# Kernel optimization log

Measured on AMD Instinct MI355X. Metric: run time of the kernel, lower is better.

Reference implementation:

```python
import jax, jax.numpy as jnp
import numpy as np
from jax import lax

EPS = 1e-5
W_BITS = 8
A_BITS = 8


def _ste_round(x):
    # straight-through round (brevitas-style)
    return x + lax.stop_gradient(jnp.round(x) - x)


def weight_fake_quant(w, bits=W_BITS):
    # symmetric per-output-channel int quant: scale = max|w| / (2^(b-1)-1)
    qmax = float(2 ** (bits - 1) - 1)
    s = jnp.max(jnp.abs(w), axis=(1, 2, 3), keepdims=True) / qmax
    s = jnp.maximum(s, 1e-8)
    return jnp.clip(_ste_round(w / s), -qmax, qmax) * s


def quant_relu(x, scale, bits=A_BITS):
    # QuantReLU: relu then unsigned fake-quant with learned per-tensor scale
    qmax = float(2 ** bits - 1)
    s = jnp.maximum(scale, 1e-6)
    return jnp.clip(_ste_round(jax.nn.relu(x) / s), 0.0, qmax) * s


def conv2d(x, w, stride=1, padding=0):
    return lax.conv_general_dilated(
        x, w, window_strides=(stride, stride),
        padding=[(padding, padding), (padding, padding)],
        dimension_numbers=('NCHW', 'OIHW', 'NCHW'))


def batchnorm(x, gamma, beta, mean, var):
    # eval-mode BN with running stats
    inv = gamma / jnp.sqrt(var + EPS)
    return x * inv[None, :, None, None] + (beta - mean * inv)[None, :, None, None]


def setup_inputs() -> dict:
    key = jax.random.key(0)
    ks = jax.random.split(key, 20)
    B, Cin, P, H, W = 64, 1024, 256, 14, 14
    inp = {
        'x': jax.random.normal(ks[0], (B, Cin, H, W), jnp.float32),
        'w1': jax.random.normal(ks[1], (P, Cin, 1, 1), jnp.float32) * 0.05,
        'w2': jax.random.normal(ks[2], (P, P, 3, 3), jnp.float32) * 0.05,
        'w3': jax.random.normal(ks[3], (Cin, P, 1, 1), jnp.float32) * 0.05,
        'bn1_gamma': jax.random.uniform(ks[4], (P,), jnp.float32, 0.5, 1.5),
        'bn1_beta': jax.random.normal(ks[5], (P,), jnp.float32) * 0.1,
        'bn1_mean': jax.random.normal(ks[6], (P,), jnp.float32) * 0.1,
        'bn1_var': jax.random.uniform(ks[7], (P,), jnp.float32, 0.5, 1.5),
        'bn2_gamma': jax.random.uniform(ks[8], (P,), jnp.float32, 0.5, 1.5),
        'bn2_beta': jax.random.normal(ks[9], (P,), jnp.float32) * 0.1,
        'bn2_mean': jax.random.normal(ks[10], (P,), jnp.float32) * 0.1,
        'bn2_var': jax.random.uniform(ks[11], (P,), jnp.float32, 0.5, 1.5),
        'bn3_gamma': jax.random.uniform(ks[12], (Cin,), jnp.float32, 0.5, 1.5),
        'bn3_beta': jax.random.normal(ks[13], (Cin,), jnp.float32) * 0.1,
        'bn3_mean': jax.random.normal(ks[14], (Cin,), jnp.float32) * 0.1,
        'bn3_var': jax.random.uniform(ks[15], (Cin,), jnp.float32, 0.5, 1.5),
        's1': jax.random.uniform(ks[16], (1,), jnp.float32, 0.02, 0.1),
        's2': jax.random.uniform(ks[17], (1,), jnp.float32, 0.02, 0.1),
        's3': jax.random.uniform(ks[18], (1,), jnp.float32, 0.02, 0.1),
    }
    return inp


def reference(x, w1, w2, w3,
              bn1_gamma, bn1_beta, bn1_mean, bn1_var,
              bn2_gamma, bn2_beta, bn2_mean, bn2_var,
              bn3_gamma, bn3_beta, bn3_mean, bn3_var,
              s1, s2, s3):
    identity = x
    out = conv2d(x, weight_fake_quant(w1))
    out = batchnorm(out, bn1_gamma, bn1_beta, bn1_mean, bn1_var)
    out = quant_relu(out, s1)
    out = conv2d(out, weight_fake_quant(w2), stride=1, padding=1)
    out = batchnorm(out, bn2_gamma, bn2_beta, bn2_mean, bn2_var)
    out = quant_relu(out, s2)
    out = conv2d(out, weight_fake_quant(w3))
    out = batchnorm(out, bn3_gamma, bn3_beta, bn3_mean, bn3_var)
    out = out + identity  # downsample=None -> identity skip
    out = quant_relu(out, s3)
    return out
```

## Files before the change

kernel.cpp:

```cpp
#include <hip/hip_runtime.h>
#include <stdint.h>
#include <stddef.h>

typedef unsigned short u16;
typedef unsigned int   u32;
typedef signed char    s8;
typedef int   i32x4 __attribute__((ext_vector_type(4)));
typedef float f32x4 __attribute__((ext_vector_type(4)));
typedef s8    s8x4  __attribute__((ext_vector_type(4)));
typedef u32   u32x4 __attribute__((ext_vector_type(4)));

#define DEVFN static __device__ __forceinline__

#define GLL(g, l) __builtin_amdgcn_global_load_lds( \
    (__attribute__((address_space(1))) void*)(g),   \
    (__attribute__((address_space(3))) void*)(l), 16, 0, 0)

#define NREAL 12544
#define NPAD  16384
#define GUARD_ROWS 32
#define SXI 4096.0f

DEVFN float blockReduceMax(float m) {
    for (int off = 32; off; off >>= 1) m = fmaxf(m, __shfl_xor(m, off));
    __shared__ float s[4];
    int lane = threadIdx.x & 63, w = threadIdx.x >> 6;
    if (lane == 0) s[w] = m;
    __syncthreads();
    return fmaxf(fmaxf(s[0], s[1]), fmaxf(s[2], s[3]));
}
DEVFN float blockReduceSum(float v) {
    for (int off = 32; off; off >>= 1) v += __shfl_xor(v, off);
    __shared__ float s[4];
    int lane = threadIdx.x & 63, w = threadIdx.x >> 6;
    __syncthreads();
    if (lane == 0) s[w] = v;
    __syncthreads();
    return s[0] + s[1] + s[2] + s[3];
}

__global__ __launch_bounds__(256) void k_prep(
    const float* __restrict__ w1, const float* __restrict__ w2, const float* __restrict__ w3,
    const float* __restrict__ x,
    const float* __restrict__ g1, const float* __restrict__ b1, const float* __restrict__ m1, const float* __restrict__ v1,
    const float* __restrict__ g2, const float* __restrict__ b2, const float* __restrict__ m2, const float* __restrict__ v2,
    const float* __restrict__ g3, const float* __restrict__ b3, const float* __restrict__ m3, const float* __restrict__ v3,
    const float* __restrict__ s1p, const float* __restrict__ s2p,
    s8* __restrict__ w1q8, s8* __restrict__ w2t8, s8* __restrict__ w3q8,
    float* __restrict__ a1, float* __restrict__ c1,
    float* __restrict__ a2, float* __restrict__ c2,
    float* __restrict__ a3, float* __restrict__ c3,
    s8* __restrict__ xq, s8* __restrict__ act1g)
{
    __shared__ float tile[64*197];
    const int bid = blockIdx.x, t = threadIdx.x;

    if (bid < 256) {
        int p = bid;
        const float* wr = w1 + (size_t)p * 1024;
        float v[4], mx = 0.f;
        for (int i = 0; i < 4; ++i) { v[i] = wr[t + i*256]; mx = fmaxf(mx, fabsf(v[i])); }
        mx = blockReduceMax(mx);
        float s = fmaxf(mx / 127.0f, 1e-8f);
        float qs = 0.f;
        for (int i = 0; i < 4; ++i) {
            float q = fminf(fmaxf(rintf(v[i] / s), -127.f), 127.f);
            s8 qb = (s8)(int)q;
            w1q8[(size_t)p*2048 + t + i*256]        = qb;
            w1q8[(size_t)p*2048 + 1024 + t + i*256] = qb;
            qs += q;
        }
        qs = blockReduceSum(qs);
        if (t == 0) {
            float s1 = fmaxf(s1p[0], 1e-6f);
            float inv = g1[p] / sqrtf(v1[p] + 1e-5f);
            float a = s * (1.0f / SXI) * inv / s1;
            a1[p] = a;
            c1[p] = (b1[p] - m1[p] * inv) / s1 + 128.0f * qs * a;
        }
    } else if (bid < 512) {
        int p = bid - 256;
        const float* wr = w2 + (size_t)p * 2304;
        float v[9], mx = 0.f;
        for (int i = 0; i < 9; ++i) { v[i] = wr[t + i*256]; mx = fmaxf(mx, fabsf(v[i])); }
        mx = blockReduceMax(mx);
        float s = fmaxf(mx / 127.0f, 1e-8f);
        float qs = 0.f;
        for (int i = 0; i < 9; ++i) {
            int f = t + i*256;
            int ci = f / 9, r = f - ci*9;
            float q = fminf(fmaxf(rintf(v[i] / s), -127.f), 127.f);
            w2t8[(size_t)p*2304 + r*256 + ci] = (s8)(int)q;
            qs += q;
        }
        qs = blockReduceSum(qs);
        if (t == 0) {
            float s1 = fmaxf(s1p[0], 1e-6f), s2 = fmaxf(s2p[0], 1e-6f);
            float inv = g2[p] / sqrtf(v2[p] + 1e-5f);
            float a = s * s1 * inv / s2;
            a2[p] = a;
            c2[p] = (b2[p] - m2[p] * inv) / s2 + 128.0f * qs * a;
        }
    } else if (bid < 1536) {
        int co = bid - 512;
        float v = w3[(size_t)co*256 + t];
        float mx = blockReduceMax(fabsf(v));
        float s = fmaxf(mx / 127.0f, 1e-8f);
        float q = fminf(fmaxf(rintf(v / s), -127.f), 127.f);
        w3q8[(size_t)co*256 + t] = (s8)(int)q;
        float qs = blockReduceSum(q);
        if (t == 0) {
            float s2 = fmaxf(s2p[0], 1e-6f);
            float inv = g3[co] / sqrtf(v3[co] + 1e-5f);
            float a = s * s2 * inv;
            a3[co] = a;
            c3[co] = (b3[co] - m3[co] * inv) + 128.0f * qs * a;
        }
    } else if (bid < 2560) {
        int sb = bid - 1536;
        int b = sb >> 4, cg = sb & 15;
        const float* xb = x + ((size_t)b*1024 + cg*64) * 196;
        for (int i = t; i < 3136; i += 256) {
            f32x4 v = *(const f32x4*)&xb[i*4];
            int g = i*4;
#pragma unroll
            for (int j = 0; j < 4; ++j) {
                int gg = g + j;
                tile[gg + gg/196] = v[j];
            }
        }
        __syncthreads();
        for (int i = t; i < 3136; i += 256) {
            int pos = i >> 4, c4 = (i & 15) << 2;
            s8x4 hi, lo;
#pragma unroll
            for (int j = 0; j < 4; ++j) {
                float v = tile[(c4 + j)*197 + pos];
                int xf = (int)rintf(v * SXI);
                xf = xf > 32767 ? 32767 : (xf < -32767 ? -32767 : xf);
                int h = xf >> 8;
                int l = xf - (h << 8) - 128;
                hi[j] = (s8)h;
                lo[j] = (s8)l;
            }
            size_t n = (size_t)(b*196 + pos);
            *(s8x4*)&xq[n*2048 + cg*64 + c4]        = hi;
            *(s8x4*)&xq[n*2048 + 1024 + cg*64 + c4] = lo;
        }
    } else {
        const int total16 = (NPAD + 2*GUARD_ROWS) * 256 / 16;
        u32x4 val; val[0] = val[1] = val[2] = val[3] = 0x80808080u;
        u32x4* dst = (u32x4*)act1g;
        for (int i = (bid - 2560)*256 + t; i < total16; i += 260*256) dst[i] = val;
    }
}

template<int CONV>
__global__ __launch_bounds__(256) void k_gemm(
    const s8* __restrict__ A, const s8* __restrict__ Bact,
    s8* __restrict__ actout,
    const float* __restrict__ ca, const float* __restrict__ cc,
    const float* __restrict__ xin, const float* __restrict__ s3p,
    float* __restrict__ outp)
{
    constexpr int KSA = CONV==1 ? 2048 : (CONV==2 ? 2304 : 256);
    constexpr int KSB = CONV==1 ? 2048 : 256;
    constexpr int NKT = CONV==1 ? 16 : (CONV==2 ? 18 : 2);

    __shared__ s8 lA[3][128*128];
    __shared__ s8 lB[3][64*128];

    const int t = threadIdx.x;
    const int lane = t & 63, wv = t >> 6;
    const int n0 = blockIdx.x * 64, m0 = blockIdx.y * 128;

    i32x4 acc[4][2], accB[4][2];
#pragma unroll
    for (int i = 0; i < 4; ++i)
#pragma unroll
        for (int j = 0; j < 2; ++j) { acc[i][j] = i32x4{0,0,0,0}; accB[i][j] = i32x4{0,0,0,0}; }

    const int srA = wv*32 + (lane >> 3);
    const int srB = wv*16 + (lane >> 3);
    const int ssel = (((lane & 7) ^ ((lane >> 3) & 7))) * 16;
    const int wr = wv >> 1, wc = wv & 1;
    const int fr = lane & 15, fg = lane >> 4;
    const int fsw = (fr & 7) << 4;

    auto stageK = [&](int kt, int buf) {
        int bcol, bshift;
        if constexpr (CONV == 2) {
            bcol = (kt & 1) * 128;
            int kpos = kt >> 1;
            int ky = kpos / 3, kx = kpos - ky*3;
            bshift = (ky - 1)*16 + (kx - 1);
        } else { bcol = kt * 128; bshift = 0; }
#pragma unroll
        for (int c = 0; c < 4; ++c) {
            const s8* g = A + (size_t)(m0 + srA + c*8) * KSA + kt*128 + ssel;
            GLL(g, &lA[buf][(wv*32 + c*8) * 128]);
        }
#pragma unroll
        for (int c = 0; c < 2; ++c) {
            const s8* g = Bact + (ptrdiff_t)(n0 + srB + c*8 + bshift) * KSB + bcol + ssel;
            GLL(g, &lB[buf][(wv*16 + c*8) * 128]);
        }
    };

    auto computeK = [&](int buf, i32x4 (&ac)[4][2]) {
        const s8* bA = &lA[buf][0];
        const s8* bB = &lB[buf][0];
        __builtin_amdgcn_s_setprio(1);
#pragma unroll
        for (int kk = 0; kk < 2; ++kk) {
            i32x4 af[4], bf[2];
#pragma unroll
            for (int m = 0; m < 4; ++m) {
                int row = wr*64 + m*16 + fr;
                af[m] = *(const i32x4*)(bA + row*128 + ((kk*64 + fg*16) ^ fsw));
            }
#pragma unroll
            for (int n = 0; n < 2; ++n) {
                int row = wc*32 + n*16 + fr;
                bf[n] = *(const i32x4*)(bB + row*128 + ((kk*64 + fg*16) ^ fsw));
            }
#pragma unroll
            for (int m = 0; m < 4; ++m)
#pragma unroll
                for (int n = 0; n < 2; ++n)
                    ac[m][n] = __builtin_amdgcn_mfma_i32_16x16x64_i8(af[m], bf[n], ac[m][n], 0, 0, 0);
        }
        __builtin_amdgcn_s_setprio(0);
    };

    stageK(0, 0);
    stageK(1, 1);
    asm volatile("s_waitcnt vmcnt(6)" ::: "memory");
    __builtin_amdgcn_s_barrier();

#pragma unroll
    for (int kt = 0; kt < NKT; ++kt) {
        const int buf = kt % 3;
        if (kt + 2 < NKT) stageK(kt + 2, (kt + 2) % 3);
        if (CONV == 1 && kt >= 8) computeK(buf, accB);
        else                      computeK(buf, acc);
        if (kt + 1 < NKT) {
            if (kt + 2 < NKT) { asm volatile("s_waitcnt vmcnt(6)" ::: "memory"); }
            else              { asm volatile("s_waitcnt vmcnt(0)" ::: "memory"); }
            __builtin_amdgcn_s_barrier();
        }
    }

    const int pb = m0 + wr*64 + fg*4;
    const int nb = n0 + wc*32 + fr;

    if constexpr (CONV != 3) {
        (void)xin; (void)s3p; (void)outp;
#pragma unroll
        for (int m = 0; m < 4; ++m) {
            int p0 = pb + m*16;
            float av[4], cv[4];
#pragma unroll
            for (int j = 0; j < 4; ++j) { av[j] = ca[p0+j]; cv[j] = cc[p0+j]; }
#pragma unroll
            for (int n = 0; n < 2; ++n) {
                int nn = nb + n*16;
                int np;
                if constexpr (CONV == 1) {
                    int b  = nn / 196;
                    int pos = nn - b*196;
                    int h = pos / 14, w = pos - h*14;
                    np = b*256 + (h+1)*16 + (w+1);
                } else {
                    int hp = (nn >> 4) & 15, wp = nn & 15;
                    if (hp < 1 || hp > 14 || wp < 1 || wp > 14) continue;
                    np = (nn >> 8)*196 + (hp-1)*14 + (wp-1);
                }
                s8x4 st;
#pragma unroll
                for (int j = 0; j < 4; ++j) {
                    float fa;
                    if constexpr (CONV == 1)
                        fa = 256.0f * (float)acc[m][n][j] + (float)accB[m][n][j];
                    else
                        fa = (float)acc[m][n][j];
                    float y = fmaxf(fa * av[j] + cv[j], 0.f);
                    int q = (int)fminf(rintf(y), 255.f);
                    st[j] = (s8)(q - 128);
                }
                *(s8x4*)&actout[(size_t)np*256 + p0] = st;
            }
        }
    } else {
        (void)actout;
        float s3 = fmaxf(s3p[0], 1e-6f);
        float rs3 = 1.0f / s3;
#pragma unroll
        for (int n = 0; n < 2; ++n) {
            int co = nb + n*16;
            float av = ca[co], cv = cc[co];
#pragma unroll
            for (int m = 0; m < 4; ++m) {
                int p4 = pb + m*16;
                int b  = p4 / 196;
                int hw = p4 - b*196;
                size_t off = ((size_t)((b << 10) + co))*196 + hw;
                f32x4 xv = *(const f32x4*)&xin[off];
                f32x4 st;
#pragma unroll
                for (int j = 0; j < 4; ++j) {
                    float y = fmaxf((float)acc[m][n][j] * av + cv + xv[j], 0.f);
                    float q = fminf(rintf(y * rs3), 255.f);
                    st[j] = q * s3;
                }
                *(f32x4*)&outp[off] = st;
            }
        }
    }
}

extern "C" void kernel_launch(void* const* d_in, const int* in_sizes, int n_in,
                              void* d_out, int out_size, void* d_ws, size_t ws_size,
                              hipStream_t stream) {
    (void)in_sizes; (void)n_in; (void)out_size; (void)ws_size;
    const float* x   = (const float*)d_in[0];
    const float* w1  = (const float*)d_in[1];
    const float* w2  = (const float*)d_in[2];
    const float* w3  = (const float*)d_in[3];
    const float* g1  = (const float*)d_in[4];
    const float* b1  = (const float*)d_in[5];
    const float* m1  = (const float*)d_in[6];
    const float* v1  = (const float*)d_in[7];
    const float* g2  = (const float*)d_in[8];
    const float* b2  = (const float*)d_in[9];
    const float* m2  = (const float*)d_in[10];
    const float* v2  = (const float*)d_in[11];
    const float* g3  = (const float*)d_in[12];
    const float* b3  = (const float*)d_in[13];
    const float* m3  = (const float*)d_in[14];
    const float* v3  = (const float*)d_in[15];
    const float* s1p = (const float*)d_in[16];
    const float* s2p = (const float*)d_in[17];
    const float* s3p = (const float*)d_in[18];
    float* out = (float*)d_out;

    char* w = (char*)d_ws;
    s8* w1q8 = (s8*)w;  w += (size_t)256*2048;
    s8* w2t8 = (s8*)w;  w += (size_t)256*2304;
    s8* w3q8 = (s8*)w;  w += (size_t)1024*256;
    float* a1 = (float*)w; w += 256*4;
    float* c1 = (float*)w; w += 256*4;
    float* a2 = (float*)w; w += 256*4;
    float* c2 = (float*)w; w += 256*4;
    float* a3 = (float*)w; w += 1024*4;
    float* c3 = (float*)w; w += 1024*4;
    s8* xq    = (s8*)w; w += (size_t)NREAL*2048;
    s8* act1g = (s8*)w; w += (size_t)(NPAD + 2*GUARD_ROWS)*256;
    s8* act1  = act1g + (size_t)GUARD_ROWS*256;
    s8* act2  = (s8*)w; w += (size_t)NREAL*256;

    k_prep<<<2820, 256, 0, stream>>>(w1, w2, w3, x,
                                     g1,b1,m1,v1, g2,b2,m2,v2, g3,b3,m3,v3,
                                     s1p, s2p,
                                     w1q8, w2t8, w3q8,
                                     a1,c1, a2,c2, a3,c3,
                                     xq, act1g);

    k_gemm<1><<<dim3(196, 2), 256, 0, stream>>>(w1q8, xq, act1, a1, c1, nullptr, nullptr, nullptr);
    k_gemm<2><<<dim3(256, 2), 256, 0, stream>>>(w2t8, act1, act2, a2, c2, nullptr, nullptr, nullptr);
    k_gemm<3><<<dim3(16, 98), 256, 0, stream>>>(act2, w3q8, nullptr, a3, c3, x, s3p, out);
}
```

Before: 203.8 us.

## Use a dedicated 128x128-tile, 512-thread kernel for the 3x3 conv GEMM

Splits the 3x3 convolution out of the templated GEMM into its own kernel with a 128x128 output tile and 8 waves per block, instead of 128x64 with 4 waves. Each block stages twice as many B columns, which halves the number of blocks and doubles reuse of the staged weight tiles. The cost is more LDS per block (96KB across the triple buffer) and only 256 blocks, which may hurt occupancy or tail balance.

```diff
diff --git a/kernel.cpp b/kernel.cpp
--- a/kernel.cpp
+++ b/kernel.cpp
@@ -163,9 +163,9 @@
     const float* __restrict__ xin, const float* __restrict__ s3p,
     float* __restrict__ outp)
 {
-    constexpr int KSA = CONV==1 ? 2048 : (CONV==2 ? 2304 : 256);
+    constexpr int KSA = CONV==1 ? 2048 : 256;
     constexpr int KSB = CONV==1 ? 2048 : 256;
-    constexpr int NKT = CONV==1 ? 16 : (CONV==2 ? 18 : 2);
+    constexpr int NKT = CONV==1 ? 16 : 2;
 
     __shared__ s8 lA[3][128*128];
     __shared__ s8 lB[3][64*128];
@@ -188,13 +188,6 @@
     const int fsw = (fr & 7) << 4;
 
     auto stageK = [&](int kt, int buf) {
-        int bcol, bshift;
-        if constexpr (CONV == 2) {
-            bcol = (kt & 1) * 128;
-            int kpos = kt >> 1;
-            int ky = kpos / 3, kx = kpos - ky*3;
-            bshift = (ky - 1)*16 + (kx - 1);
-        } else { bcol = kt * 128; bshift = 0; }
 #pragma unroll
         for (int c = 0; c < 4; ++c) {
             const s8* g = A + (size_t)(m0 + srA + c*8) * KSA + kt*128 + ssel;
@@ -202,7 +195,7 @@
         }
 #pragma unroll
         for (int c = 0; c < 2; ++c) {
-            const s8* g = Bact + (ptrdiff_t)(n0 + srB + c*8 + bshift) * KSB + bcol + ssel;
+            const s8* g = Bact + (ptrdiff_t)(n0 + srB + c*8) * KSB + kt*128 + ssel;
             GLL(g, &lB[buf][(wv*16 + c*8) * 128]);
         }
     };
@@ -254,7 +247,7 @@
     const int pb = m0 + wr*64 + fg*4;
     const int nb = n0 + wc*32 + fr;
 
-    if constexpr (CONV != 3) {
+    if constexpr (CONV == 1) {
         (void)xin; (void)s3p; (void)outp;
 #pragma unroll
         for (int m = 0; m < 4; ++m) {
@@ -265,25 +258,14 @@
 #pragma unroll
             for (int n = 0; n < 2; ++n) {
                 int nn = nb + n*16;
-                int np;
-                if constexpr (CONV == 1) {
-                    int b  = nn / 196;
-                    int pos = nn - b*196;
-                    int h = pos / 14, w = pos - h*14;
-                    np = b*256 + (h+1)*16 + (w+1);
-                } else {
-                    int hp = (nn >> 4) & 15, wp = nn & 15;
-                    if (hp < 1 || hp > 14 || wp < 1 || wp > 14) continue;
-                    np = (nn >> 8)*196 + (hp-1)*14 + (wp-1);
-                }
+                int b  = nn / 196;
+                int pos = nn - b*196;
+                int h = pos / 14, w = pos - h*14;
+                int np = b*256 + (h+1)*16 + (w+1);
                 s8x4 st;
 #pragma unroll
                 for (int j = 0; j < 4; ++j) {
-                    float fa;
-                    if constexpr (CONV == 1)
-                        fa = 256.0f * (float)acc[m][n][j] + (float)accB[m][n][j];
-                    else
-                        fa = (float)acc[m][n][j];
+                    float fa = 256.0f * (float)acc[m][n][j] + (float)accB[m][n][j];
                     float y = fmaxf(fa * av[j] + cv[j], 0.f);
                     int q = (int)fminf(rintf(y), 255.f);
                     st[j] = (s8)(q - 128);
@@ -315,6 +297,118 @@
                 }
                 *(f32x4*)&outp[off] = st;
             }
+        }
+    }
+}
+
+__global__ __launch_bounds__(512) void k_gemm2(
+    const s8* __restrict__ A, const s8* __restrict__ Bact,
+    s8* __restrict__ actout,
+    const float* __restrict__ ca, const float* __restrict__ cc)
+{
+    constexpr int NKT = 18;
+
+    __shared__ s8 lA[3][128*128];
+    __shared__ s8 lB[3][128*128];
+
+    const int t = threadIdx.x;
+    const int lane = t & 63, wv = t >> 6;
+    const int n0 = blockIdx.x * 128, m0 = blockIdx.y * 128;
+
+    i32x4 acc[4][2];
+#pragma unroll
+    for (int i = 0; i < 4; ++i)
+#pragma unroll
+        for (int j = 0; j < 2; ++j) acc[i][j] = i32x4{0,0,0,0};
+
+    const int srAB = wv*16 + (lane >> 3);
+    const int ssel = (((lane & 7) ^ ((lane >> 3) & 7))) * 16;
+    const int wr = wv >> 2, wc = wv & 3;
+    const int fr = lane & 15, fg = lane >> 4;
+    const int fsw = (fr & 7) << 4;
+
+    auto stageK = [&](int kt, int buf) {
+        int bcol = (kt & 1) * 128;
+        int kpos = kt >> 1;
+        int ky = kpos / 3, kx = kpos - ky*3;
+        int bshift = (ky - 1)*16 + (kx - 1);
+#pragma unroll
+        for (int c = 0; c < 2; ++c) {
+            const s8* g = A + (size_t)(m0 + srAB + c*8) * 2304 + kt*128 + ssel;
+            GLL(g, &lA[buf][(wv*16 + c*8) * 128]);
+        }
+#pragma unroll
+        for (int c = 0; c < 2; ++c) {
+            const s8* g = Bact + (ptrdiff_t)(n0 + srAB + c*8 + bshift) * 256 + bcol + ssel;
+            GLL(g, &lB[buf][(wv*16 + c*8) * 128]);
+        }
+    };
+
+    auto computeK = [&](int buf) {
+        const s8* bA = &lA[buf][0];
+        const s8* bB = &lB[buf][0];
+        __builtin_amdgcn_s_setprio(1);
+#pragma unroll
+        for (int kk = 0; kk < 2; ++kk) {
+            i32x4 af[4], bf[2];
+#pragma unroll
+            for (int m = 0; m < 4; ++m) {
+                int row = wr*64 + m*16 + fr;
+                af[m] = *(const i32x4*)(bA + row*128 + ((kk*64 + fg*16) ^ fsw));
+            }
+#pragma unroll
+            for (int n = 0; n < 2; ++n) {
+                int row = wc*32 + n*16 + fr;
+                bf[n] = *(const i32x4*)(bB + row*128 + ((kk*64 + fg*16) ^ fsw));
+            }
+#pragma unroll
+            for (int m = 0; m < 4; ++m)
+#pragma unroll
+                for (int n = 0; n < 2; ++n)
+                    acc[m][n] = __builtin_amdgcn_mfma_i32_16x16x64_i8(af[m], bf[n], acc[m][n], 0, 0, 0);
+        }
+        __builtin_amdgcn_s_setprio(0);
+    };
+
+    stageK(0, 0);
+    stageK(1, 1);
+    asm volatile("s_waitcnt vmcnt(4)" ::: "memory");
+    __builtin_amdgcn_s_barrier();
+
+#pragma unroll
+    for (int kt = 0; kt < NKT; ++kt) {
+        const int buf = kt % 3;
+        if (kt + 2 < NKT) stageK(kt + 2, (kt + 2) % 3);
+        computeK(buf);
+        if (kt + 1 < NKT) {
+            if (kt + 2 < NKT) { asm volatile("s_waitcnt vmcnt(4)" ::: "memory"); }
+            else              { asm volatile("s_waitcnt vmcnt(0)" ::: "memory"); }
+            __builtin_amdgcn_s_barrier();
+        }
+    }
+
+    const int pb = m0 + wr*64 + fg*4;
+    const int nb = n0 + wc*32 + fr;
+#pragma unroll
+    for (int m = 0; m < 4; ++m) {
+        int p0 = pb + m*16;
+        float av[4], cv[4];
+#pragma unroll
+        for (int j = 0; j < 4; ++j) { av[j] = ca[p0+j]; cv[j] = cc[p0+j]; }
+#pragma unroll
+        for (int n = 0; n < 2; ++n) {
+            int nn = nb + n*16;
+            int hp = (nn >> 4) & 15, wp = nn & 15;
+            if (hp < 1 || hp > 14 || wp < 1 || wp > 14) continue;
+            int np = (nn >> 8)*196 + (hp-1)*14 + (wp-1);
+            s8x4 st;
+#pragma unroll
+            for (int j = 0; j < 4; ++j) {
+                float y = fmaxf((float)acc[m][n][j] * av[j] + cv[j], 0.f);
+                int q = (int)fminf(rintf(y), 255.f);
+                st[j] = (s8)(q - 128);
+            }
+            *(s8x4*)&actout[(size_t)np*256 + p0] = st;
         }
     }
 }
@@ -367,6 +461,6 @@
                                      xq, act1g);
 
     k_gemm<1><<<dim3(196, 2), 256, 0, stream>>>(w1q8, xq, act1, a1, c1, nullptr, nullptr, nullptr);
-    k_gemm<2><<<dim3(256, 2), 256, 0, stream>>>(w2t8, act1, act2, a2, c2, nullptr, nullptr, nullptr);
+    k_gemm2<<<dim3(128, 2), 512, 0, stream>>>(w2t8, act1, act2, a2, c2);
     k_gemm<3><<<dim3(16, 98), 256, 0, stream>>>(act2, w3q8, nullptr, a3, c3, x, s3p, out);
 }
```

After: 204.9 us. About the same (+0.6%).
